# Kernel tuning notes

Measured on AMD Instinct MI355X. Metric: run time of the kernel, lower is better.

## Reference

```python
import jax, jax.numpy as jnp
import numpy as np


def setup_inputs() -> dict:
    key = jax.random.key(0)
    k1, k2 = jax.random.split(key)
    B, C, H, W = 8, 256, 128, 128
    query = jax.random.normal(k1, (B, C, H, W), dtype=jnp.float32)
    target = jax.random.normal(k2, (B, C, H, W), dtype=jnp.float32)
    # torch.randperm(64) permutations, made deterministic for the reference
    idx1 = jnp.arange(64, dtype=jnp.int64)
    idx2 = jnp.arange(64, dtype=jnp.int64)
    return {"query": query, "target": target, "idx1": idx1, "idx2": idx2}


def reference(query, target, idx1, idx2):
    # dist term: 1 - per-spatial-position channel dot product.
    # Original does this via millions of degenerate 1xCx1 bmm calls on
    # transposed [B,W,H,C] views; the math is an elementwise-mul + channel reduce.
    dist = 1.0 - jnp.einsum('bchw,bchw->bwh', query, target)  # [B,W,H]

    # random-sample similarity term
    B, C, H, W = target.shape
    target_spatially_flat = target.reshape(B, C * H, W)  # flatten(1,2)
    num_samples = min(C * H, 64)  # == 64 here
    randomly_sampled = target_spatially_flat[:, idx1[:num_samples]]        # [B,64,W]
    another_random_sample = target_spatially_flat[:, idx2[:num_samples]]   # [B,64,W]
    # bmm of [B*64,1,W] with flip-over-batch [B*64,W,1] -> per-pair dot over W
    flipped = jnp.flip(another_random_sample, axis=0)
    random_similarity = jnp.einsum('bnw,bnw->bn', randomly_sampled, flipped)  # [B,64]

    return dist.mean() + jnp.maximum(random_similarity, 0.0).mean()
```

## Files before the change

kernel.cpp:

```cpp
#include <hip/hip_runtime.h>

#define B_ 8
#define C_ 256
#define H_ 128
#define W_ 128
#define N_TOTAL (B_ * C_ * H_ * W_)
#define N_VEC   (N_TOTAL / 4)
#define NB1     2048
#define NT1     256
#define NSAMP   64
#define NB2     (B_ * NSAMP)

__global__ __launch_bounds__(NT1) void dot_partial_kernel(
    const float4* __restrict__ q, const float4* __restrict__ t,
    float* __restrict__ partial) {
    int tid = blockIdx.x * NT1 + threadIdx.x;
    int stride = gridDim.x * NT1;
    float acc = 0.0f;
    for (int i = tid; i < N_VEC; i += stride) {
        float4 a = q[i];
        float4 b = t[i];
        acc += a.x * b.x + a.y * b.y + a.z * b.z + a.w * b.w;
    }
    #pragma unroll
    for (int off = 32; off > 0; off >>= 1) acc += __shfl_down(acc, off, 64);
    __shared__ float s[NT1 / 64];
    int wid = threadIdx.x >> 6;
    int lane = threadIdx.x & 63;
    if (lane == 0) s[wid] = acc;
    __syncthreads();
    if (threadIdx.x == 0) {
        float blocksum = 0.0f;
        #pragma unroll
        for (int w = 0; w < NT1 / 64; ++w) blocksum += s[w];
        partial[blockIdx.x] = blocksum;
    }
}

__global__ __launch_bounds__(64) void sim_kernel(
    const float* __restrict__ t, const int* __restrict__ idx1,
    const int* __restrict__ idx2, float* __restrict__ partial) {
    int blk = blockIdx.x;
    int b = blk >> 6;
    int n = blk & (NSAMP - 1);
    int i1 = idx1[n];
    int i2 = idx2[n];
    const float* p1 = t + ((size_t)b * (C_ * H_) + i1) * W_;
    const float* p2 = t + ((size_t)(B_ - 1 - b) * (C_ * H_) + i2) * W_;
    int lane = threadIdx.x;
    float acc = p1[lane] * p2[lane] + p1[lane + 64] * p2[lane + 64];
    #pragma unroll
    for (int off = 32; off > 0; off >>= 1) acc += __shfl_down(acc, off, 64);
    if (lane == 0) partial[blk] = fmaxf(acc, 0.0f);
}

__global__ __launch_bounds__(256) void finalize_kernel(
    const float* __restrict__ p1, const float* __restrict__ p2,
    float* __restrict__ out) {
    float a = 0.0f;
    for (int i = threadIdx.x; i < NB1; i += 256) a += p1[i];
    float b = 0.0f;
    for (int i = threadIdx.x; i < NB2; i += 256) b += p2[i];
    #pragma unroll
    for (int off = 32; off > 0; off >>= 1) {
        a += __shfl_down(a, off, 64);
        b += __shfl_down(b, off, 64);
    }
    __shared__ float sa[4], sb[4];
    int wid = threadIdx.x >> 6;
    int lane = threadIdx.x & 63;
    if (lane == 0) { sa[wid] = a; sb[wid] = b; }
    __syncthreads();
    if (threadIdx.x == 0) {
        float A = sa[0] + sa[1] + sa[2] + sa[3];
        float Bs = sb[0] + sb[1] + sb[2] + sb[3];
        out[0] = 1.0f - A / (float)(B_ * H_ * W_) + Bs / (float)NB2;
    }
}

extern "C" void kernel_launch(void* const* d_in, const int* in_sizes, int n_in,
                              void* d_out, int out_size, void* d_ws, size_t ws_size,
                              hipStream_t stream) {
    const float* query  = (const float*)d_in[0];
    const float* target = (const float*)d_in[1];
    const int*   idx1   = (const int*)d_in[2];
    const int*   idx2   = (const int*)d_in[3];
    float* out = (float*)d_out;

    float* partial1 = (float*)d_ws;
    float* partial2 = partial1 + NB1;

    dot_partial_kernel<<<NB1, NT1, 0, stream>>>(
        (const float4*)query, (const float4*)target, partial1);
    sim_kernel<<<NB2, 64, 0, stream>>>(target, idx1, idx2, partial2);
    finalize_kernel<<<1, 256, 0, stream>>>(partial1, partial2, out);
}
```

Baseline: 51.93 us.

## Fuse sim kernel into main dot-product kernel and unroll with nontemporal loads

Folds the sampled-similarity computation into the first 512 blocks of the main streaming dot-product kernel, removing one kernel launch. The grid-stride loop becomes a fully unrolled fixed-trip loop with four independent accumulators and four loads in flight per iteration. Query loads use nontemporal hints so they do not pollute the cache. Target loads stay normal, so the similarity rows may still hit in cache. The added branch and extra loads in early blocks can add slight imbalance.

```diff
diff --git a/kernel.cpp b/kernel.cpp
--- a/kernel.cpp
+++ b/kernel.cpp
@@ -8,20 +8,51 @@
 #define N_VEC   (N_TOTAL / 4)
 #define NB1     2048
 #define NT1     256
+#define GSTRIDE (NB1 * NT1)
+#define ITERS   (N_VEC / GSTRIDE)
 #define NSAMP   64
 #define NB2     (B_ * NSAMP)
 
-__global__ __launch_bounds__(NT1) void dot_partial_kernel(
-    const float4* __restrict__ q, const float4* __restrict__ t,
-    float* __restrict__ partial) {
-    int tid = blockIdx.x * NT1 + threadIdx.x;
-    int stride = gridDim.x * NT1;
-    float acc = 0.0f;
-    for (int i = tid; i < N_VEC; i += stride) {
-        float4 a = q[i];
-        float4 b = t[i];
-        acc += a.x * b.x + a.y * b.y + a.z * b.z + a.w * b.w;
+typedef float f4 __attribute__((ext_vector_type(4)));
+
+__global__ __launch_bounds__(NT1) void fused_main_kernel(
+    const f4* __restrict__ q, const f4* __restrict__ t,
+    const int* __restrict__ idx1, const int* __restrict__ idx2,
+    float* __restrict__ partial1, float* __restrict__ partial2) {
+    int blk = blockIdx.x;
+
+    if (blk < NB2 && threadIdx.x < 64) {
+        const float* tf = (const float*)t;
+        int b = blk >> 6;
+        int n = blk & (NSAMP - 1);
+        const float* p1 = tf + ((size_t)b * (C_ * H_) + idx1[n]) * W_;
+        const float* p2 = tf + ((size_t)(B_ - 1 - b) * (C_ * H_) + idx2[n]) * W_;
+        int lane = threadIdx.x;
+        float acc = p1[lane] * p2[lane] + p1[lane + 64] * p2[lane + 64];
+        #pragma unroll
+        for (int off = 32; off > 0; off >>= 1) acc += __shfl_down(acc, off, 64);
+        if (lane == 0) partial2[blk] = fmaxf(acc, 0.0f);
     }
+
+    int tid = blk * NT1 + threadIdx.x;
+    float acc0 = 0.f, acc1 = 0.f, acc2 = 0.f, acc3 = 0.f;
+    #pragma unroll
+    for (int j = 0; j < ITERS; j += 4) {
+        f4 qa = __builtin_nontemporal_load(q + tid + (size_t)(j + 0) * GSTRIDE);
+        f4 qb = __builtin_nontemporal_load(q + tid + (size_t)(j + 1) * GSTRIDE);
+        f4 qc = __builtin_nontemporal_load(q + tid + (size_t)(j + 2) * GSTRIDE);
+        f4 qd = __builtin_nontemporal_load(q + tid + (size_t)(j + 3) * GSTRIDE);
+        f4 ta = t[tid + (size_t)(j + 0) * GSTRIDE];
+        f4 tb = t[tid + (size_t)(j + 1) * GSTRIDE];
+        f4 tc = t[tid + (size_t)(j + 2) * GSTRIDE];
+        f4 td = t[tid + (size_t)(j + 3) * GSTRIDE];
+        acc0 += qa.x * ta.x + qa.y * ta.y + qa.z * ta.z + qa.w * ta.w;
+        acc1 += qb.x * tb.x + qb.y * tb.y + qb.z * tb.z + qb.w * tb.w;
+        acc2 += qc.x * tc.x + qc.y * tc.y + qc.z * tc.z + qc.w * tc.w;
+        acc3 += qd.x * td.x + qd.y * td.y + qd.z * td.z + qd.w * td.w;
+    }
+    float acc = (acc0 + acc1) + (acc2 + acc3);
+
     #pragma unroll
     for (int off = 32; off > 0; off >>= 1) acc += __shfl_down(acc, off, 64);
     __shared__ float s[NT1 / 64];
@@ -33,25 +64,8 @@
         float blocksum = 0.0f;
         #pragma unroll
         for (int w = 0; w < NT1 / 64; ++w) blocksum += s[w];
-        partial[blockIdx.x] = blocksum;
+        partial1[blk] = blocksum;
     }
-}
-
-__global__ __launch_bounds__(64) void sim_kernel(
-    const float* __restrict__ t, const int* __restrict__ idx1,
-    const int* __restrict__ idx2, float* __restrict__ partial) {
-    int blk = blockIdx.x;
-    int b = blk >> 6;
-    int n = blk & (NSAMP - 1);
-    int i1 = idx1[n];
-    int i2 = idx2[n];
-    const float* p1 = t + ((size_t)b * (C_ * H_) + i1) * W_;
-    const float* p2 = t + ((size_t)(B_ - 1 - b) * (C_ * H_) + i2) * W_;
-    int lane = threadIdx.x;
-    float acc = p1[lane] * p2[lane] + p1[lane + 64] * p2[lane + 64];
-    #pragma unroll
-    for (int off = 32; off > 0; off >>= 1) acc += __shfl_down(acc, off, 64);
-    if (lane == 0) partial[blk] = fmaxf(acc, 0.0f);
 }
 
 __global__ __launch_bounds__(256) void finalize_kernel(
@@ -72,7 +86,7 @@
     if (lane == 0) { sa[wid] = a; sb[wid] = b; }
     __syncthreads();
     if (threadIdx.x == 0) {
-        float A = sa[0] + sa[1] + sa[2] + sa[3];
+        float A  = sa[0] + sa[1] + sa[2] + sa[3];
         float Bs = sb[0] + sb[1] + sb[2] + sb[3];
         out[0] = 1.0f - A / (float)(B_ * H_ * W_) + Bs / (float)NB2;
     }
@@ -90,8 +104,8 @@
     float* partial1 = (float*)d_ws;
     float* partial2 = partial1 + NB1;
 
-    dot_partial_kernel<<<NB1, NT1, 0, stream>>>(
-        (const float4*)query, (const float4*)target, partial1);
-    sim_kernel<<<NB2, 64, 0, stream>>>(target, idx1, idx2, partial2);
+    fused_main_kernel<<<NB1, NT1, 0, stream>>>(
+        (const f4*)query, (const f4*)target, idx1, idx2,
+        partial1, partial2);
     finalize_kernel<<<1, 256, 0, stream>>>(partial1, partial2, out);
 }
```

Measured after the change: 54.19 us. 1.04x slower.
